# Optimization experiments

Measured on AMD Instinct MI355X. Metric: run time of the kernel, lower is better.

Reference implementation:

```python
import jax, jax.numpy as jnp
import numpy as np

COMMITMENT_WEIGHT = 0.25


def _vq_layer(residual, codebook):
    """One euclidean VQ layer: nearest-codeword lookup + straight-through.
    residual: [B,T,D], codebook: [K,D].
    Returns (q_st [B,T,D], idx [B,T], commit_loss scalar).
    """
    B, T, D = residual.shape
    flat = residual.reshape(-1, D)  # [N,D]
    d2 = (jnp.sum(flat * flat, axis=-1, keepdims=True)
          - 2.0 * flat @ codebook.T
          + jnp.sum(codebook * codebook, axis=-1))  # [N,K]
    idx = jnp.argmin(d2, axis=-1)                   # [N]
    q = codebook[idx].reshape(B, T, D)
    # straight-through estimator (as in vector_quantize_pytorch)
    q_st = residual + jax.lax.stop_gradient(q - residual)
    commit_loss = COMMITMENT_WEIGHT * jnp.mean(
        (jax.lax.stop_gradient(q) - residual) ** 2)
    return q_st, idx.reshape(B, T), commit_loss


def setup_inputs() -> dict:
    key = jax.random.key(0)
    ks = jax.random.split(key, 9)
    D = 768
    sizes = [2, 4, 8, 16, 32, 64, 128, 256]
    inp = {"x": jax.random.normal(ks[0], (32, 2048, D), dtype=jnp.float32)}
    for i, K in enumerate(sizes):
        inp[f"cb{i}"] = jax.random.normal(ks[i + 1], (K, D), dtype=jnp.float32)
    return inp


def reference(x, cb0, cb1, cb2, cb3, cb4, cb5, cb6, cb7):
    codebooks = [cb0, cb1, cb2, cb3, cb4, cb5, cb6, cb7]
    residual = x
    quantized = jnp.zeros_like(x)
    all_indices = []
    total_commit_loss = jnp.float32(0.0)
    for cb in codebooks:  # fixed 8 structurally-distinct layers
        q, idx, commit = _vq_layer(residual, cb)
        quantized = quantized + q
        residual = residual - q
        all_indices.append(idx)
        total_commit_loss = total_commit_loss + commit
    all_indices = jnp.stack(all_indices, axis=-1)  # [B,T,num_layers]
    return quantized, all_indices, total_commit_loss
```

## Files before the change

### kernel.cpp

```cpp
#include <hip/hip_runtime.h>
#include <stdint.h>

#define NTOK 65536
#define DIM  768
#define NCB  512
#define NC   510
#define TAU  0.75f

typedef _Float16 f16x8 __attribute__((ext_vector_type(8)));
typedef float f32x4 __attribute__((ext_vector_type(4)));

#define WS_C32   0u
#define WS_CHI   1572864u
#define WS_CNORM 3145728u
#define WS_G     3147776u
#define WS_IDX   4196352u
#define WS_PART  6293504u
#define WS_XN    6match_placeholder
#undef WS_XN
#define WS_XN    6359040u
#define WS_S     8388608u
#define S_BYTES  67108864u

__device__ __forceinline__ void gl_lds16(const void* g, void* l){
  __builtin_amdgcn_global_load_lds(
      (const __attribute__((address_space(1))) unsigned int*)g,
      (__attribute__((address_space(3))) unsigned int*)l,
      16, 0, 0);
}

__global__ void k_prep(const float* __restrict__ cb0, const float* __restrict__ cb1,
                       const float* __restrict__ cb2, const float* __restrict__ cb3,
                       const float* __restrict__ cb4, const float* __restrict__ cb5,
                       const float* __restrict__ cb6, const float* __restrict__ cb7,
                       char* __restrict__ ws){
  const int r = blockIdx.x, t = threadIdx.x;
  const float* srcs[8] = {cb0,cb1,cb2,cb3,cb4,cb5,cb6,cb7};
  const int off[8] = {0,2,6,14,30,62,126,254};
  const int KK[8]  = {2,4,8,16,32,64,128,256};
  const float* src = nullptr;
#pragma unroll
  for (int l=0;l<8;l++)
    if (r >= off[l] && r < off[l]+KK[l]) src = srcs[l] + (size_t)(r - off[l]) * DIM;
  float* C32 = (float*)(ws + WS_C32);
  _Float16* Chi = (_Float16*)(ws + WS_CHI);
  double ss = 0.0;
#pragma unroll
  for (int i=0;i<3;i++){
    const int e = t + i*256;
    const float v = src ? src[e] : 0.f;
    C32[(size_t)r*DIM + e] = v;
    Chi[(size_t)r*DIM + e] = (_Float16)v;
    ss += (double)v * (double)v;
  }
  __shared__ double red[256];
  red[t] = ss; __syncthreads();
  for (int sdown=128; sdown>0; sdown>>=1){
    if (t < sdown) red[t] += red[t+sdown];
    __syncthreads();
  }
  if (t == 0){
    float* cnp = (float*)(ws + WS_CNORM);
    cnp[r] = (r < NC) ? (float)red[0] : 1e30f;
  }
}

__global__ void k_gram(char* __restrict__ ws){
  const int i = blockIdx.x, t = threadIdx.x;
  const float* __restrict__ C32 = (const float*)(ws + WS_C32);
  __shared__ float row[DIM];
  for (int e=t; e<DIM; e+=256) row[e] = C32[(size_t)i*DIM + e];
  __syncthreads();
  float* __restrict__ G = (float*)(ws + WS_G);
  for (int j=t; j<NCB; j+=256){
    const float4* cj = (const float4*)(C32 + (size_t)j*DIM);
    double d = 0.0;
    for (int k=0; k<DIM/4; k++){
      const float4 b = cj[k];
      d += (double)row[4*k]*(double)b.x + (double)row[4*k+1]*(double)b.y
         + (double)row[4*k+2]*(double)b.z + (double)row[4*k+3]*(double)b.w;
    }
    G[(size_t)i*NCB + j] = (float)d;
  }
}

__global__ __launch_bounds__(256, 3) void k_gemm(const float* __restrict__ x,
                                                 const char* __restrict__ ws,
                                                 _Float16* __restrict__ S,
                                                 float* __restrict__ xn){
  __shared__ __align__(16) char smem[49152];
  const int t = threadIdx.x, lane = t & 63, w = t >> 6;
  const int wm = w >> 1, wn = w & 1;
  const int bid = blockIdx.x;
  const int xcd = bid & 7, jj = bid >> 3;
  const int mt = xcd*64 + (jj >> 2), nt = jj & 3;
  const _Float16* __restrict__ Chi = (const _Float16*)(ws + WS_CHI);

  f32x4 acc[4][4];
#pragma unroll
  for (int i=0;i<4;i++)
#pragma unroll
    for (int j=0;j<4;j++) acc[i][j] = {0.f,0.f,0.f,0.f};

  float xs = 0.f;

  for (int kt=0; kt<12; kt++){
#pragma unroll
    for (int i8=0;i8<8;i8++){
      const int r0 = w*32 + i8*4;
      const int row = r0 + (lane>>4);
      const int g = lane & 15;
      const int sg = g ^ (((row&7)<<1) | ((row>>3)&1));
      const size_t go = (size_t)(mt*128 + row)*DIM + (size_t)kt*64 + sg*4;
      gl_lds16(x + go, smem + r0*256);
    }
#pragma unroll
    for (int c4=0;c4<4;c4++){
      const int r0 = w*32 + c4*8;
      const int rloc = r0 + (lane>>3);
      const int jsrc = (lane&7) ^ (rloc&7);
      const size_t go = (size_t)(nt*128 + rloc)*DIM + (size_t)kt*64 + jsrc*8;
      gl_lds16(Chi + go, smem + 32768 + r0*128);
    }
    __syncthreads();
    if (nt == 0){
      const int rr = t & 127, hf = t >> 7;
#pragma unroll
      for (int g=0; g<8; g++){
        const f32x4 v = *(const f32x4*)(smem + rr*256 + hf*128 + g*16);
        xs += v[0]*v[0] + v[1]*v[1] + v[2]*v[2] + v[3]*v[3];
      }
    }
#pragma unroll
    for (int kk=0; kk<2; kk++){
      f16x8 fa[4], fb[4];
#pragma unroll
      for (int mf=0;mf<4;mf++){
        const int m = wm*64 + mf*16 + (lane&15);
        const int maskm = ((m&7)<<1) | ((m>>3)&1);
        const int ch = kk*4 + (lane>>4);
        const int g0 = (2*ch) ^ maskm;
        const f32x4 lo = *(const f32x4*)(smem + m*256 + g0*16);
        const f32x4 hi = *(const f32x4*)(smem + m*256 + (g0^1)*16);
        f16x8 r;
        r[0]=(_Float16)lo[0]; r[1]=(_Float16)lo[1]; r[2]=(_Float16)lo[2]; r[3]=(_Float16)lo[3];
        r[4]=(_Float16)hi[0]; r[5]=(_Float16)hi[1]; r[6]=(_Float16)hi[2]; r[7]=(_Float16)hi[3];
        fa[mf] = r;
      }
#pragma unroll
      for (int nf=0;nf<4;nf++){
        const int c = wn*64 + nf*16 + (lane&15);
        const uint bb = (uint)(32768 + c*128 + ((((kk<<2)+(lane>>4)) ^ (c&7))*16));
        fb[nf] = *(const f16x8*)(smem + bb);
      }
#pragma unroll
      for (int mf=0;mf<4;mf++)
#pragma unroll
        for (int nf=0;nf<4;nf++)
          acc[mf][nf] = __builtin_amdgcn_mfma_f32_16x16x32_f16(fa[mf], fb[nf], acc[mf][nf], 0,0,0);
    }
    __syncthreads();
  }

  if (nt == 0){
    ((float*)smem)[t] = xs;
    __syncthreads();
    if (t < 128) xn[mt*128 + t] = ((float*)smem)[t] + ((float*)smem)[t + 128];
  }

#pragma unroll
  for (int mf=0;mf<4;mf++)
#pragma unroll
    for (int nf=0;nf<4;nf++){
      const f32x4 v = acc[mf][nf];
      const int col  = nt*128 + wn*64 + nf*16 + (lane&15);
      const int row0 = mt*128 + wm*64 + mf*16 + ((lane>>4)<<2);
#pragma unroll
      for (int e=0;e<4;e++)
        S[(size_t)(row0+e)*NCB + col] = (_Float16)v[e];
    }
}

template<int FUSED>
__global__ __launch_bounds__(256, 4) void k_chain(const float* __restrict__ x,
                                                  const _Float16* __restrict__ S,
                                                  char* __restrict__ ws,
                                                  float* __restrict__ out,
                                                  float* __restrict__ part,
                                                  const float* __restrict__ xn){
  const int t = threadIdx.x, lane = t & 63, w = t >> 6;
  const size_t tok = (size_t)blockIdx.x*4 + w;
  const float* __restrict__ cn  = (const float*)(ws + WS_CNORM);
  const float* __restrict__ G   = (const float*)(ws + WS_G);
  const float* __restrict__ C32 = (const float*)(ws + WS_C32);

  float sv[8], s0[8], cnv[8];
  {
    const uint* sp = (const uint*)(S + tok*NCB);
#pragma unroll
    for (int j=0;j<4;j++){
      union { uint u; _Float16 h[2]; } cv;
      cv.u = sp[j*64 + lane];
      sv[2*j]   = (float)cv.h[0];
      sv[2*j+1] = (float)cv.h[1];
      const float2 c2 = *(const float2*)(cn + j*128 + lane*2);
      cnv[2*j] = c2.x; cnv[2*j+1] = c2.y;
    }
  }
#pragma unroll
  for (int k=0;k<8;k++) s0[k] = sv[k];

  int mcs[8];
  float h = FUSED ? xn[tok] : 0.f;
  float tot = 0.f;

#pragma unroll
  for (int l=0; l<8; ++l){
    const int cs = (2<<l) - 2;
    const int ce = cs + (2<<l);
    float bv = 3e38f; int bc = 0x7fffffff;
#pragma unroll
    for (int j=0;j<4;j++){
      const int c0 = j*128 + lane*2;
      const float sA = (c0   >= cs && c0   < ce) ? (cnv[2*j]   - 2.f*sv[2*j])   : 3e38f;
      const float sB = (c0+1 >= cs && c0+1 < ce) ? (cnv[2*j+1] - 2.f*sv[2*j+1]) : 3e38f;
      if (sA < bv){ bv = sA; bc = c0; }
      if (sB < bv){ bv = sB; bc = c0+1; }
    }
#pragma unroll
    for (int d=1; d<64; d<<=1){
      const float ov = __shfl_xor(bv, d);
      const int   oc = __shfl_xor(bc, d);
      if (ov < bv || (ov == bv && oc < bc)){ bv = ov; bc = oc; }
    }
    int bm = 0;
#pragma unroll
    for (int j=0;j<4;j++){
      const int c0 = j*128 + lane*2;
      const float sA = (c0   >= cs && c0   < ce) ? (cnv[2*j]   - 2.f*sv[2*j])   : 3e38f;
      const float sB = (c0+1 >= cs && c0+1 < ce) ? (cnv[2*j+1] - 2.f*sv[2*j+1]) : 3e38f;
      if (sA <= bv + TAU) bm |= 1 << (2*j);
      if (sB <= bv + TAU) bm |= 1 << (2*j+1);
    }
    const unsigned long long lmask = __ballot(bm != 0);
    const int b0 = __ffsll((long long)lmask) - 1;
    const int bm0 = __shfl(bm, b0);
    const bool multi = (__popcll(lmask) > 1) || ((bm0 & (bm0-1)) != 0);

    int mc = bc;
    float ssel = bv;
    if (multi){
      float xv[12];
      {
        const float4* xp = (const float4*)(x + tok*DIM + lane*12);
#pragma unroll
        for (int q=0;q<3;q++){
          const float4 v = xp[q];
          xv[q*4]=v.x; xv[q*4+1]=v.y; xv[q*4+2]=v.z; xv[q*4+3]=v.w;
        }
      }
      double bve = 1e300; int bce = 0x7fffffff;
      unsigned long long Lm = lmask;
      while (Lm){
        const int b = __ffsll((long long)Lm) - 1; Lm &= Lm - 1;
        const int mbits = __shfl(bm, b);
#pragma unroll
        for (int k=0;k<8;k++){
          if (mbits & (1<<k)){
            const int c = (k>>1)*128 + b*2 + (k&1);
            const float dkv = __shfl(s0[k] - sv[k], b);
            const float* __restrict__ crow = C32 + (size_t)c*DIM + lane*12;
            double dd = 0.0;
#pragma unroll
            for (int q=0;q<3;q++){
              const float4 v = *(const float4*)(crow + q*4);
              dd += (double)xv[q*4]*v.x + (double)xv[q*4+1]*v.y
                  + (double)xv[q*4+2]*v.z + (double)xv[q*4+3]*v.w;
            }
#pragma unroll
            for (int d=1; d<64; d<<=1) dd += __shfl_xor(dd, d);
            const double se = (double)cn[c] - 2.0*(dd - (double)dkv);
            if (se < bve || (se == bve && c < bce)){ bve = se; bce = c; }
          }
        }
      }
      mc = bce;
      ssel = (float)bve;
    }
    mcs[l] = mc;
    if (FUSED){ h += ssel; tot += h; }
    if (l < 7){
      const float* __restrict__ gr = G + (size_t)mc*NCB;
#pragma unroll
      for (int j=0;j<4;j++){
        const float2 g2 = *(const float2*)(gr + j*128 + lane*2);
        sv[2*j] -= g2.x; sv[2*j+1] -= g2.y;
      }
    }
  }

  if (FUSED){
    float q[12];
#pragma unroll
    for (int i=0;i<12;i++) q[i] = 0.f;
#pragma unroll
    for (int l=0;l<8;l++){
      const float* __restrict__ cw = C32 + (size_t)mcs[l]*DIM + lane*12;
#pragma unroll
      for (int qq=0;qq<3;qq++){
        const float4 v = *(const float4*)(cw + qq*4);
        q[qq*4]+=v.x; q[qq*4+1]+=v.y; q[qq*4+2]+=v.z; q[qq*4+3]+=v.w;
      }
    }
    float* op = out + tok*DIM + lane*12;
#pragma unroll
    for (int qq=0;qq<3;qq++){
      float4 v; v.x=q[qq*4]; v.y=q[qq*4+1]; v.z=q[qq*4+2]; v.w=q[qq*4+3];
      *(float4*)(op + qq*4) = v;
    }
    if (lane == 0){
      float4 i0, i1;
      i0.x=(float)(mcs[0]-0);   i0.y=(float)(mcs[1]-2);   i0.z=(float)(mcs[2]-6);   i0.w=(float)(mcs[3]-14);
      i1.x=(float)(mcs[4]-30);  i1.y=(float)(mcs[5]-62);  i1.z=(float)(mcs[6]-126); i1.w=(float)(mcs[7]-254);
      *(float4*)(out + (size_t)NTOK*DIM + tok*8)     = i0;
      *(float4*)(out + (size_t)NTOK*DIM + tok*8 + 4) = i1;
    }
    __shared__ float bs[4];
    if (lane == 0) bs[w] = tot;
    __syncthreads();
    if (t == 0) part[blockIdx.x] = bs[0]+bs[1]+bs[2]+bs[3];
  } else {
    if (lane == 0){
      int* idxw = (int*)(ws + WS_IDX);
      const int offs[8] = {0,2,6,14,30,62,126,254};
#pragma unroll
      for (int l=0;l<8;l++) idxw[tok*8 + l] = mcs[l] - offs[l];
    }
  }
}

__global__ __launch_bounds__(512) void k_fin(const float* __restrict__ x,
                                             char* __restrict__ ws,
                                             float* __restrict__ out,
                                             float* __restrict__ part){
  const int t = threadIdx.x, lane = t & 63, w = t >> 6;
  const size_t tok = (size_t)blockIdx.x * 8 + w;
  const int off[8] = {0,2,6,14,30,62,126,254};
  const int* __restrict__ idxw = (const int*)(ws + WS_IDX);
  const float* __restrict__ C32 = (const float*)(ws + WS_C32);
  int loc[8];
#pragma unroll
  for (int l=0;l<8;l++) loc[l] = idxw[tok*8 + l];
  if (lane < 8) out[(size_t)NTOK*DIM + tok*8 + lane] = (float)idxw[tok*8 + lane];

  const float4* __restrict__ xr = (const float4*)(x + tok*DIM);
  float4* __restrict__ qr = (float4*)(out + tok*DIM);
  const float4* crow[8];
#pragma unroll
  for (int l=0;l<8;l++) crow[l] = (const float4*)(C32 + (size_t)(loc[l] + off[l])*DIM);
  float ssq = 0.f;
#pragma unroll
  for (int i=0;i<3;i++){
    const int e4 = i*64 + lane;
    const float4 xv = xr[e4];
    float rx = xv.x, ry = xv.y, rz = xv.z, rw = xv.w;
    float qx = 0.f, qy = 0.f, qz = 0.f, qw = 0.f;
#pragma unroll
    for (int l=0;l<8;l++){
      const float4 cv = crow[l][e4];
      rx -= cv.x; ry -= cv.y; rz -= cv.z; rw -= cv.w;
      qx += cv.x; qy += cv.y; qz += cv.z; qw += cv.w;
      ssq += rx*rx + ry*ry + rz*rz + rw*rw;
    }
    float4 q; q.x = qx; q.y = qy; q.z = qz; q.w = qw;
    qr[e4] = q;
  }
#pragma unroll
  for (int d=32; d>0; d>>=1) ssq += __shfl_down(ssq, d);
  __shared__ float bsum[8];
  if (lane == 0) bsum[w] = ssq;
  __syncthreads();
  if (t == 0){
    float s2 = 0.f;
#pragma unroll
    for (int j=0;j<8;j++) s2 += bsum[j];
    part[blockIdx.x] = s2;
  }
}

__global__ void k_loss(const float* __restrict__ part, int n,
                       float* __restrict__ out){
  const int t = threadIdx.x;
  double s = 0.0;
  for (int i=t; i<n; i+=256) s += (double)part[i];
  __shared__ double red[256];
  red[t] = s; __syncthreads();
  for (int d=128; d>0; d>>=1){
    if (t < d) red[t] += red[t+d];
    __syncthreads();
  }
  if (t == 0)
    out[(size_t)NTOK*DIM + (size_t)NTOK*8] =
      (float)(0.25 * red[0] / (double)((size_t)NTOK * DIM));
}

extern "C" void kernel_launch(void* const* d_in, const int* in_sizes, int n_in,
                              void* d_out, int out_size, void* d_ws, size_t ws_size,
                              hipStream_t stream){
  const float* x = (const float*)d_in[0];
  char* ws = (char*)d_ws;
  float* out = (float*)d_out;
  float* part = (float*)(ws + WS_PART);
  float* xn   = (float*)(ws + WS_XN);
  const bool fused = ws_size >= (size_t)WS_S + (size_t)S_BYTES;
  _Float16* Sp = fused ? (_Float16*)(ws + WS_S) : (_Float16*)out;

  k_prep<<<512, 256, 0, stream>>>((const float*)d_in[1], (const float*)d_in[2],
                                  (const float*)d_in[3], (const float*)d_in[4],
                                  (const float*)d_in[5], (const float*)d_in[6],
                                  (const float*)d_in[7], (const float*)d_in[8], ws);
  k_gram<<<512, 256, 0, stream>>>(ws);
  k_gemm<<<2048, 256, 0, stream>>>(x, ws, Sp, xn);
  if (fused){
    k_chain<1><<<16384, 256, 0, stream>>>(x, Sp, ws, out, part, xn);
    k_loss<<<1, 256, 0, stream>>>(part, 16384, out);
  } else {
    k_chain<0><<<16384, 256, 0, stream>>>(x, Sp, ws, out, part, xn);
    k_fin<<<8192, 512, 0, stream>>>(x, ws, out, part);
    k_loss<<<1, 256, 0, stream>>>(part, 8192, out);
  }
}
```

Before: 448.6 us.

## Double-buffer GEMM with fp16 A staging, pack argmin keys, widen chain blocks

The GEMM now loads x rows into registers, converts them to fp16 and writes them into a double-buffered, swizzled LDS tile, while the codebook tile for the next k-step is prefetched asynchronously. This halves the A-tile LDS footprint per stage and overlaps global loads with MFMA work, at the cost of occupancy (launch bounds drop from 3 to 2 blocks per CU with 64KB of shared memory). The chain kernel packs the distance value and the code index into one sortable 32-bit key, so the wave argmin needs one shuffle per step instead of two. This truncates the low bits of the distance, which the TAU-margin exact fallback must absorb. Chain blocks also grow to 512 threads handling 8 tokens each.

```diff
diff --git a/kernel.cpp b/kernel.cpp
--- a/kernel.cpp
+++ b/kernel.cpp
@@ -16,8 +16,6 @@
 #define WS_G     3147776u
 #define WS_IDX   4196352u
 #define WS_PART  6293504u
-#define WS_XN    6match_placeholder
-#undef WS_XN
 #define WS_XN    6359040u
 #define WS_S     8388608u
 #define S_BYTES  67108864u
@@ -84,11 +82,11 @@
   }
 }
 
-__global__ __launch_bounds__(256, 3) void k_gemm(const float* __restrict__ x,
+__global__ __launch_bounds__(256, 2) void k_gemm(const float* __restrict__ x,
                                                  const char* __restrict__ ws,
                                                  _Float16* __restrict__ S,
                                                  float* __restrict__ xn){
-  __shared__ __align__(16) char smem[49152];
+  __shared__ __align__(16) char smem[65536];
   const int t = threadIdx.x, lane = t & 63, w = t >> 6;
   const int wm = w >> 1, wn = w & 1;
   const int bid = blockIdx.x;
@@ -102,55 +100,57 @@
 #pragma unroll
     for (int j=0;j<4;j++) acc[i][j] = {0.f,0.f,0.f,0.f};
 
+  const int ar = t & 127, hh = t >> 7;
+  const float* __restrict__ xrow = x + (size_t)(mt*128 + ar)*DIM + hh*32;
+
+  float4 va[8];
   float xs = 0.f;
 
-  for (int kt=0; kt<12; kt++){
-#pragma unroll
-    for (int i8=0;i8<8;i8++){
-      const int r0 = w*32 + i8*4;
-      const int row = r0 + (lane>>4);
-      const int g = lane & 15;
-      const int sg = g ^ (((row&7)<<1) | ((row>>3)&1));
-      const size_t go = (size_t)(mt*128 + row)*DIM + (size_t)kt*64 + sg*4;
-      gl_lds16(x + go, smem + r0*256);
-    }
+  auto loadA = [&](int kt){
+    const float4* p = (const float4*)(xrow + (size_t)kt*64);
+#pragma unroll
+    for (int q=0;q<8;q++) va[q] = p[q];
+  };
+  auto writeA = [&](uint base){
+#pragma unroll
+    for (int q=0;q<4;q++){
+      const float4 v0 = va[2*q], v1 = va[2*q+1];
+      f16x8 hv;
+      hv[0]=(_Float16)v0.x; hv[1]=(_Float16)v0.y; hv[2]=(_Float16)v0.z; hv[3]=(_Float16)v0.w;
+      hv[4]=(_Float16)v1.x; hv[5]=(_Float16)v1.y; hv[6]=(_Float16)v1.z; hv[7]=(_Float16)v1.w;
+      const uint wb = base + (uint)(ar*128 + (((hh*4+q) ^ (ar&7))*16));
+      *(f16x8*)(smem + wb) = hv;
+    }
+    if (nt == 0){
+#pragma unroll
+      for (int q=0;q<8;q++)
+        xs += va[q].x*va[q].x + va[q].y*va[q].y + va[q].z*va[q].z + va[q].w*va[q].w;
+    }
+  };
+  auto stageB = [&](int kt, uint base){
 #pragma unroll
     for (int c4=0;c4<4;c4++){
       const int r0 = w*32 + c4*8;
       const int rloc = r0 + (lane>>3);
       const int jsrc = (lane&7) ^ (rloc&7);
       const size_t go = (size_t)(nt*128 + rloc)*DIM + (size_t)kt*64 + jsrc*8;
-      gl_lds16(Chi + go, smem + 32768 + r0*128);
-    }
-    __syncthreads();
-    if (nt == 0){
-      const int rr = t & 127, hf = t >> 7;
-#pragma unroll
-      for (int g=0; g<8; g++){
-        const f32x4 v = *(const f32x4*)(smem + rr*256 + hf*128 + g*16);
-        xs += v[0]*v[0] + v[1]*v[1] + v[2]*v[2] + v[3]*v[3];
-      }
-    }
+      gl_lds16(Chi + go, smem + base + r0*128);
+    }
+  };
+  auto compute = [&](uint abase, uint bbase){
 #pragma unroll
     for (int kk=0; kk<2; kk++){
       f16x8 fa[4], fb[4];
 #pragma unroll
       for (int mf=0;mf<4;mf++){
         const int m = wm*64 + mf*16 + (lane&15);
-        const int maskm = ((m&7)<<1) | ((m>>3)&1);
-        const int ch = kk*4 + (lane>>4);
-        const int g0 = (2*ch) ^ maskm;
-        const f32x4 lo = *(const f32x4*)(smem + m*256 + g0*16);
-        const f32x4 hi = *(const f32x4*)(smem + m*256 + (g0^1)*16);
-        f16x8 r;
-        r[0]=(_Float16)lo[0]; r[1]=(_Float16)lo[1]; r[2]=(_Float16)lo[2]; r[3]=(_Float16)lo[3];
-        r[4]=(_Float16)hi[0]; r[5]=(_Float16)hi[1]; r[6]=(_Float16)hi[2]; r[7]=(_Float16)hi[3];
-        fa[mf] = r;
+        const uint ab = abase + (uint)(m*128 + ((((kk<<2)+(lane>>4)) ^ (m&7))*16));
+        fa[mf] = *(const f16x8*)(smem + ab);
       }
 #pragma unroll
       for (int nf=0;nf<4;nf++){
         const int c = wn*64 + nf*16 + (lane&15);
-        const uint bb = (uint)(32768 + c*128 + ((((kk<<2)+(lane>>4)) ^ (c&7))*16));
+        const uint bb = bbase + (uint)(c*128 + ((((kk<<2)+(lane>>4)) ^ (c&7))*16));
         fb[nf] = *(const f16x8*)(smem + bb);
       }
 #pragma unroll
@@ -159,6 +159,22 @@
         for (int nf=0;nf<4;nf++)
           acc[mf][nf] = __builtin_amdgcn_mfma_f32_16x16x32_f16(fa[mf], fb[nf], acc[mf][nf], 0,0,0);
     }
+  };
+
+  loadA(0);
+  stageB(0, 32768u);
+  writeA(0u);
+  __syncthreads();
+
+  for (int kt=0; kt<12; kt++){
+    const uint cur = (uint)(kt & 1);
+    const uint nxt = cur ^ 1u;
+    if (kt < 11){
+      loadA(kt+1);
+      stageB(kt+1, 32768u + nxt*16384u);
+    }
+    compute(cur*16384u, 32768u + cur*16384u);
+    if (kt < 11) writeA(nxt*16384u);
     __syncthreads();
   }
 
@@ -182,14 +198,14 @@
 }
 
 template<int FUSED>
-__global__ __launch_bounds__(256, 4) void k_chain(const float* __restrict__ x,
+__global__ __launch_bounds__(512, 8) void k_chain(const float* __restrict__ x,
                                                   const _Float16* __restrict__ S,
                                                   char* __restrict__ ws,
                                                   float* __restrict__ out,
                                                   float* __restrict__ part,
                                                   const float* __restrict__ xn){
   const int t = threadIdx.x, lane = t & 63, w = t >> 6;
-  const size_t tok = (size_t)blockIdx.x*4 + w;
+  const size_t tok = (size_t)blockIdx.x*8 + w;
   const float* __restrict__ cn  = (const float*)(ws + WS_CNORM);
   const float* __restrict__ G   = (const float*)(ws + WS_G);
   const float* __restrict__ C32 = (const float*)(ws + WS_C32);
@@ -218,7 +234,7 @@
   for (int l=0; l<8; ++l){
     const int cs = (2<<l) - 2;
     const int ce = cs + (2<<l);
-    float bv = 3e38f; int bc = 0x7fffffff;
+    float bv = 3e38f; int bc = 511;
 #pragma unroll
     for (int j=0;j<4;j++){
       const int c0 = j*128 + lane*2;
@@ -227,28 +243,35 @@
       if (sA < bv){ bv = sA; bc = c0; }
       if (sB < bv){ bv = sB; bc = c0+1; }
     }
+    uint u = __float_as_uint(bv);
+    u ^= (u & 0x80000000u) ? 0xFFFFFFFFu : 0x80000000u;
+    uint key = (u & 0xFFFFFE00u) | ((uint)bc & 511u);
 #pragma unroll
     for (int d=1; d<64; d<<=1){
-      const float ov = __shfl_xor(bv, d);
-      const int   oc = __shfl_xor(bc, d);
-      if (ov < bv || (ov == bv && oc < bc)){ bv = ov; bc = oc; }
-    }
+      const uint ok = (uint)__shfl_xor((int)key, d);
+      key = (ok < key) ? ok : key;
+    }
+    const int mc0 = (int)(key & 511u);
+    const uint vq = key & 0xFFFFFE00u;
+    const uint sb = (vq & 0x80000000u) ? (vq ^ 0x80000000u) : ~vq;
+    const float bv_est = __uint_as_float(sb);
+
     int bm = 0;
 #pragma unroll
     for (int j=0;j<4;j++){
       const int c0 = j*128 + lane*2;
       const float sA = (c0   >= cs && c0   < ce) ? (cnv[2*j]   - 2.f*sv[2*j])   : 3e38f;
       const float sB = (c0+1 >= cs && c0+1 < ce) ? (cnv[2*j+1] - 2.f*sv[2*j+1]) : 3e38f;
-      if (sA <= bv + TAU) bm |= 1 << (2*j);
-      if (sB <= bv + TAU) bm |= 1 << (2*j+1);
+      if (sA <= bv_est + TAU) bm |= 1 << (2*j);
+      if (sB <= bv_est + TAU) bm |= 1 << (2*j+1);
     }
     const unsigned long long lmask = __ballot(bm != 0);
     const int b0 = __ffsll((long long)lmask) - 1;
     const int bm0 = __shfl(bm, b0);
     const bool multi = (__popcll(lmask) > 1) || ((bm0 & (bm0-1)) != 0);
 
-    int mc = bc;
-    float ssel = bv;
+    int mc = mc0;
+    float ssel = bv_est;
     if (multi){
       float xv[12];
       {
@@ -325,10 +348,15 @@
       *(float4*)(out + (size_t)NTOK*DIM + tok*8)     = i0;
       *(float4*)(out + (size_t)NTOK*DIM + tok*8 + 4) = i1;
     }
-    __shared__ float bs[4];
+    __shared__ float bs[8];
     if (lane == 0) bs[w] = tot;
     __syncthreads();
-    if (t == 0) part[blockIdx.x] = bs[0]+bs[1]+bs[2]+bs[3];
+    if (t == 0){
+      float s2 = 0.f;
+#pragma unroll
+      for (int j=0;j<8;j++) s2 += bs[j];
+      part[blockIdx.x] = s2;
+    }
   } else {
     if (lane == 0){
       int* idxw = (int*)(ws + WS_IDX);
@@ -422,10 +450,10 @@
   k_gram<<<512, 256, 0, stream>>>(ws);
   k_gemm<<<2048, 256, 0, stream>>>(x, ws, Sp, xn);
   if (fused){
-    k_chain<1><<<16384, 256, 0, stream>>>(x, Sp, ws, out, part, xn);
-    k_loss<<<1, 256, 0, stream>>>(part, 16384, out);
+    k_chain<1><<<8192, 512, 0, stream>>>(x, Sp, ws, out, part, xn);
+    k_loss<<<1, 256, 0, stream>>>(part, 8192, out);
   } else {
-    k_chain<0><<<16384, 256, 0, stream>>>(x, Sp, ws, out, part, xn);
+    k_chain<0><<<8192, 512, 0, stream>>>(x, Sp, ws, out, part, xn);
     k_fin<<<8192, 512, 0, stream>>>(x, ws, out, part);
     k_loss<<<1, 256, 0, stream>>>(part, 8192, out);
   }
```

Result: slower. 814.0 us (+81.4%).
